# Kernel optimization log

Hardware: AMD Instinct MI355X
Metric: run time of the kernel (lower is better)

## Reference

```python
import jax, jax.numpy as jnp
import numpy as np

NUM_HEADS = 16
D_MODEL = 1024
D_K = D_MODEL // NUM_HEADS
B, S = 2, 2048


def setup_inputs() -> dict:
    key = jax.random.key(0)
    ks = jax.random.split(key, 10)
    q = jax.random.normal(ks[0], (B, S, D_MODEL), dtype=jnp.float32)
    k = jax.random.normal(ks[1], (B, S, D_MODEL), dtype=jnp.float32)
    v = jax.random.normal(ks[2], (B, S, D_MODEL), dtype=jnp.float32)
    # causal mask, 1 = keep, 0 = masked (masked_fill(mask==0, -1e9))
    mask = jnp.tril(jnp.ones((S, S), dtype=jnp.int32))[None, None, :, :]
    # Linear weights ~ N(0, 0.02); biases left at torch default-ish small uniform
    std = 0.02
    Wq = jax.random.normal(ks[3], (D_MODEL, D_MODEL), dtype=jnp.float32) * std
    Wk = jax.random.normal(ks[4], (D_MODEL, D_MODEL), dtype=jnp.float32) * std
    Wv = jax.random.normal(ks[5], (D_MODEL, D_MODEL), dtype=jnp.float32) * std
    bound = 1.0 / np.sqrt(D_MODEL)
    bq = jax.random.uniform(ks[6], (D_MODEL,), jnp.float32, -bound, bound)
    bk = jax.random.uniform(ks[7], (D_MODEL,), jnp.float32, -bound, bound)
    bv = jax.random.uniform(ks[8], (D_MODEL,), jnp.float32, -bound, bound)
    return {"q": q, "k": k, "v": v, "mask": mask,
            "Wq": Wq, "bq": bq, "Wk": Wk, "bk": bk, "Wv": Wv, "bv": bv}


def reference(q, k, v, mask, Wq, bq, Wk, bk, Wv, bv):
    # projections (torch Linear: x @ W.T + b), split heads -> [B, H, S, Dk]
    def proj(x, W, b):
        y = x @ W.T + b
        return y.reshape(B, S, NUM_HEADS, D_K).transpose(0, 2, 1, 3)

    qh, kh, vh = proj(q, Wq, bq), proj(k, Wk, bk), proj(v, Wv, bv)
    scores = jnp.einsum('bhqd,bhkd->bhqk', qh, kh) / jnp.sqrt(jnp.float32(D_K))
    scores = jnp.where(mask == 0, jnp.float32(-1e9), scores)
    p = jax.nn.softmax(scores, axis=-1)
    # dropout is identity in eval mode
    x = jnp.einsum('bhqk,bhkd->bhqd', p, vh)  # [B, H, S, Dk]
    return x.transpose(0, 2, 1, 3).reshape(B, S, D_MODEL)
```

## Files before the change

kernel.cpp:

```cpp
#include <hip/hip_runtime.h>

#define B_ 2
#define H_ 16
#define S_ 2048
#define DM 1024
#define DK 64
#define NX (4096 * 1024)
#define NW (1024 * 1024)
#define NO (32 * 2048 * 64)

typedef unsigned short u16;
typedef unsigned int u32;
typedef __attribute__((ext_vector_type(8))) short bf16x8;
typedef __attribute__((ext_vector_type(8))) unsigned short u16x8;
typedef __attribute__((ext_vector_type(4))) float f32x4;

__device__ inline u16 f2bf(float f) {
  union { float f; u32 u; } c; c.f = f;
  u32 u = c.u;
  u += 0x7fffu + ((u >> 16) & 1u);
  return (u16)(u >> 16);
}
__device__ inline float bf2f(u16 v) {
  union { u32 u; float f; } c; c.u = ((u32)v) << 16;
  return c.f;
}

__device__ inline u16x8 cvt8(const float* __restrict__ src) {
  const float4 a = *reinterpret_cast<const float4*>(src);
  const float4 b = *reinterpret_cast<const float4*>(src + 4);
  u16x8 r;
  r[0] = f2bf(a.x); r[1] = f2bf(a.y); r[2] = f2bf(a.z); r[3] = f2bf(a.w);
  r[4] = f2bf(b.x); r[5] = f2bf(b.y); r[6] = f2bf(b.z); r[7] = f2bf(b.w);
  return r;
}

__device__ inline void glds16(const u16* g, u16* l) {
  __builtin_amdgcn_global_load_lds(
      (const __attribute__((address_space(1))) unsigned int*)g,
      (__attribute__((address_space(3))) unsigned int*)l, 16, 0, 0);
}

__global__ __launch_bounds__(256) void cvt_kernel(
    const float* __restrict__ q, const float* __restrict__ k, const float* __restrict__ v,
    const float* __restrict__ Wq, const float* __restrict__ Wk, const float* __restrict__ Wv,
    u16* __restrict__ Xq, u16* __restrict__ Xk, u16* __restrict__ Xv,
    u16* __restrict__ Wqb, u16* __restrict__ Wkb, u16* __restrict__ Wvb)
{
  const int t = blockIdx.y;
  const float* src = (t == 0) ? q : (t == 1) ? k : (t == 2) ? v
                   : (t == 3) ? Wq : (t == 4) ? Wk : Wv;
  u16* dst = (t == 0) ? Xq : (t == 1) ? Xk : (t == 2) ? Xv
           : (t == 3) ? Wqb : (t == 4) ? Wkb : Wvb;
  const int n = (t < 3) ? NX : NW;
  const int idx = (blockIdx.x * 256 + threadIdx.x) * 8;
  if (idx >= n) return;
  *reinterpret_cast<u16x8*>(&dst[idx]) = cvt8(&src[idx]);
}

__global__ __launch_bounds__(256) void proj_kernel(
    const u16* __restrict__ Xq, const u16* __restrict__ Xk, const u16* __restrict__ Xv,
    const u16* __restrict__ Wqb, const u16* __restrict__ Wkb, const u16* __restrict__ Wvb,
    const float* __restrict__ bq, const float* __restrict__ bk, const float* __restrict__ bv,
    u16* __restrict__ Qh, u16* __restrict__ Kh, u16* __restrict__ Vh)
{
  const int z = blockIdx.z;
  const u16* X      = (z == 0) ? Xq : (z == 1) ? Xk : Xv;
  const u16* W      = (z == 0) ? Wqb : (z == 1) ? Wkb : Wvb;
  const float* bias = (z == 0) ? bq : (z == 1) ? bk : bv;
  u16* out          = (z == 0) ? Qh : (z == 1) ? Kh : Vh;
  const float scale = (z == 0) ? 0.18033688f : 1.0f;

  __shared__ __align__(16) u16 Xs[128 * 64];
  __shared__ __align__(16) u16 Ws[128 * 64];

  const int tid = threadIdx.x;
  const int lane = tid & 63;
  const int w = tid >> 6;
  const int wy = w >> 1, wx = w & 1;
  const int m0 = blockIdx.y * 128;
  const int n0 = blockIdx.x * 128;
  const int ml = lane & 15;
  const int qd = lane >> 4;

  f32x4 acc[4][4] = {};

  for (int kb = 0; kb < DM; kb += 64) {
    __syncthreads();
    #pragma unroll
    for (int p = 0; p < 4; ++p) {
      const int c = p * 4 + w;
      const int row = c * 8 + (lane >> 3);
      const int col = kb + (lane & 7) * 8;
      glds16(&X[(size_t)(m0 + row) * DM + col], &Xs[c * 512]);
      glds16(&W[(size_t)(n0 + row) * DM + col], &Ws[c * 512]);
    }
    __syncthreads();
    bf16x8 a[4][2], bfr[4][2];
    #pragma unroll
    for (int i = 0; i < 4; ++i)
      #pragma unroll
      for (int kc = 0; kc < 2; ++kc)
        a[i][kc] = *reinterpret_cast<const bf16x8*>(&Xs[(wy * 64 + i * 16 + ml) * 64 + kc * 32 + qd * 8]);
    #pragma unroll
    for (int j = 0; j < 4; ++j)
      #pragma unroll
      for (int kc = 0; kc < 2; ++kc)
        bfr[j][kc] = *reinterpret_cast<const bf16x8*>(&Ws[(wx * 64 + j * 16 + ml) * 64 + kc * 32 + qd * 8]);
    #pragma unroll
    for (int i = 0; i < 4; ++i)
      #pragma unroll
      for (int j = 0; j < 4; ++j) {
        acc[i][j] = __builtin_amdgcn_mfma_f32_16x16x32_bf16(a[i][0], bfr[j][0], acc[i][j], 0, 0, 0);
        acc[i][j] = __builtin_amdgcn_mfma_f32_16x16x32_bf16(a[i][1], bfr[j][1], acc[i][j], 0, 0, 0);
      }
  }

  #pragma unroll
  for (int j = 0; j < 4; ++j) {
    const int n = n0 + wx * 64 + j * 16 + ml;
    const float badd = bias[n];
    const int h = n >> 6, d = n & 63;
    #pragma unroll
    for (int i = 0; i < 4; ++i) {
      #pragma unroll
      for (int r = 0; r < 4; ++r) {
        const int m = m0 + wy * 64 + i * 16 + qd * 4 + r;
        const int bi = m >> 11, s = m & 2047;
        out[((bi * H_ + h) * S_ + s) * DK + d] = f2bf((acc[i][j][r] + badd) * scale);
      }
    }
  }
}

__global__ __launch_bounds__(256) void transpose_kernel(
    const u16* __restrict__ Vh, u16* __restrict__ Vt)
{
  __shared__ __align__(16) u16 T[64 * 72];
  const int t = threadIdx.x;
  const int st = blockIdx.x, bh = blockIdx.y;
  {
    const int r = t >> 2, c = (t & 3) * 16;
    const u16* src = &Vh[((size_t)bh * S_ + st * 64 + r) * DK + c];
    *reinterpret_cast<u16x8*>(&T[r * 72 + c])     = *reinterpret_cast<const u16x8*>(src);
    *reinterpret_cast<u16x8*>(&T[r * 72 + c + 8]) = *reinterpret_cast<const u16x8*>(src + 8);
  }
  __syncthreads();
  {
    const int d = t >> 2, s0 = (t & 3) * 16;
    u16x8 a, b;
    #pragma unroll
    for (int i = 0; i < 8; ++i) a[i] = T[(s0 + i) * 72 + d];
    #pragma unroll
    for (int i = 0; i < 8; ++i) b[i] = T[(s0 + 8 + i) * 72 + d];
    u16* dst = &Vt[((size_t)bh * DK + d) * S_ + st * 64 + s0];
    *reinterpret_cast<u16x8*>(dst)     = a;
    *reinterpret_cast<u16x8*>(dst + 8) = b;
  }
}

__global__ __launch_bounds__(256) void attn_kernel(
    const u16* __restrict__ Qh, const u16* __restrict__ Kh,
    const u16* __restrict__ Vt, u16* __restrict__ Op, float* __restrict__ lp)
{
  __shared__ __align__(16) u16 Ks[64 * 72];
  __shared__ __align__(16) u16 Vs[64 * 72];
  __shared__ __align__(16) u16 Ps[4 * 16 * 72];

  const int tid  = threadIdx.x;
  const int lane = tid & 63;
  const int w    = tid >> 6;
  const int qt   = 31 - blockIdx.x;
  const int bh   = blockIdx.y;
  const int half = blockIdx.z;
  const int nt   = qt + 1;
  const int na   = (nt + 1) >> 1;
  const int t0   = half ? na : 0;
  const int t1   = half ? nt : na;
  const int ml   = lane & 15, qd = lane >> 4;
  const int R0   = qt * 64 + w * 16;

  bf16x8 qa[2];
  #pragma unroll
  for (int ch = 0; ch < 2; ++ch)
    qa[ch] = *reinterpret_cast<const bf16x8*>(
        &Qh[((size_t)bh * S_ + R0 + ml) * DK + ch * 32 + qd * 8]);

  f32x4 oacc[4] = {};
  float l = 0.f;

  const u16* kbase = Kh + (size_t)bh * S_ * DK;
  const u16* vbase = Vt + (size_t)bh * DK * S_;
  u16* pw = &Ps[w * 16 * 72 + ml * 72];

  const int sr = tid >> 3;
  const int sc = (tid & 7) * 8;

  float4 kr0 = *reinterpret_cast<const float4*>(&kbase[(size_t)(t0 * 64 + sr) * DK + sc]);
  float4 kr1 = *reinterpret_cast<const float4*>(&kbase[(size_t)(t0 * 64 + sr + 32) * DK + sc]);
  float4 vr0 = *reinterpret_cast<const float4*>(&vbase[(size_t)sr * S_ + t0 * 64 + sc]);
  float4 vr1 = *reinterpret_cast<const float4*>(&vbase[(size_t)(sr + 32) * S_ + t0 * 64 + sc]);

  for (int t = t0; t < t1; ++t) {
    __syncthreads();
    *reinterpret_cast<float4*>(&Ks[sr * 72 + sc])        = kr0;
    *reinterpret_cast<float4*>(&Ks[(sr + 32) * 72 + sc]) = kr1;
    *reinterpret_cast<float4*>(&Vs[sr * 72 + sc])        = vr0;
    *reinterpret_cast<float4*>(&Vs[(sr + 32) * 72 + sc]) = vr1;
    __syncthreads();

    if (t + 1 < t1) {
      const int tn = t + 1;
      kr0 = *reinterpret_cast<const float4*>(&kbase[(size_t)(tn * 64 + sr) * DK + sc]);
      kr1 = *reinterpret_cast<const float4*>(&kbase[(size_t)(tn * 64 + sr + 32) * DK + sc]);
      vr0 = *reinterpret_cast<const float4*>(&vbase[(size_t)sr * S_ + tn * 64 + sc]);
      vr1 = *reinterpret_cast<const float4*>(&vbase[(size_t)(sr + 32) * S_ + tn * 64 + sc]);
    }

    const bool diag = (t == qt);
    const int jmax = diag ? w : 3;

    f32x4 sfr[4];
    #pragma unroll
    for (int j = 0; j < 4; ++j) {
      if (j > jmax) break;
      f32x4 zz = {};
      #pragma unroll
      for (int ch = 0; ch < 2; ++ch) {
        bf16x8 kb = *reinterpret_cast<const bf16x8*>(&Ks[(j * 16 + ml) * 72 + ch * 32 + qd * 8]);
        zz = __builtin_amdgcn_mfma_f32_16x16x32_bf16(kb, qa[ch], zz, 0, 0, 0);
      }
      sfr[j] = zz;
    }

    if (diag) {
      #pragma unroll
      for (int r = 0; r < 4; ++r)
        if (qd * 4 + r > ml) sfr[jmax][r] = -1e30f;
    }

    #pragma unroll
    for (int j = 0; j < 4; ++j) {
      u32 p0 = 0, p1 = 0;
      if (j <= jmax) {
        union { float f; u32 u; } e0, e1, e2, e3;
        e0.f = __builtin_amdgcn_exp2f(sfr[j][0]);
        e1.f = __builtin_amdgcn_exp2f(sfr[j][1]);
        e2.f = __builtin_amdgcn_exp2f(sfr[j][2]);
        e3.f = __builtin_amdgcn_exp2f(sfr[j][3]);
        l += (e0.f + e1.f) + (e2.f + e3.f);
        p0 = __builtin_amdgcn_perm(e1.u, e0.u, 0x07060302u);
        p1 = __builtin_amdgcn_perm(e3.u, e2.u, 0x07060302u);
      }
      u32* pd = reinterpret_cast<u32*>(&pw[j * 16 + qd * 4]);
      pd[0] = p0; pd[1] = p1;
    }

    const int chmax = (diag && w < 2) ? 0 : 1;
    #pragma unroll
    for (int ch = 0; ch < 2; ++ch) {
      if (ch > chmax) break;
      bf16x8 pa = *reinterpret_cast<const bf16x8*>(&Ps[w * 16 * 72 + ml * 72 + ch * 32 + qd * 8]);
      #pragma unroll
      for (int dj = 0; dj < 4; ++dj) {
        bf16x8 vb = *reinterpret_cast<const bf16x8*>(&Vs[(dj * 16 + ml) * 72 + ch * 32 + qd * 8]);
        oacc[dj] = __builtin_amdgcn_mfma_f32_16x16x32_bf16(pa, vb, oacc[dj], 0, 0, 0);
      }
    }
  }

  l += __shfl_xor(l, 16, 64);
  l += __shfl_xor(l, 32, 64);
  const size_t rbase = (size_t)(half * 32 + bh) * S_;
  if (qd == 0) lp[rbase + R0 + ml] = l;
  #pragma unroll
  for (int dj = 0; dj < 4; ++dj)
    #pragma unroll
    for (int r = 0; r < 4; ++r)
      Op[(rbase + R0 + qd * 4 + r) * DK + dj * 16 + ml] = f2bf(oacc[dj][r]);
}

__global__ __launch_bounds__(256) void merge_kernel(
    const u16* __restrict__ Op, const float* __restrict__ lp,
    float* __restrict__ out)
{
  const int idx8 = (blockIdx.x * 256 + threadIdx.x) * 8;
  const int row = idx8 >> 6;
  const int d = idx8 & 63;
  const float inv = 1.f / (lp[row] + lp[row + 32 * S_]);
  const u16x8 a = *reinterpret_cast<const u16x8*>(&Op[idx8]);
  const u16x8 c = *reinterpret_cast<const u16x8*>(&Op[(size_t)idx8 + NO]);
  const int bh = row >> 11, s = row & 2047;
  const int b = bh >> 4, h = bh & 15;
  float* dst = &out[(size_t)(b * S_ + s) * DM + h * DK + d];
  float4 o0, o1;
  o0.x = (bf2f(a[0]) + bf2f(c[0])) * inv;
  o0.y = (bf2f(a[1]) + bf2f(c[1])) * inv;
  o0.z = (bf2f(a[2]) + bf2f(c[2])) * inv;
  o0.w = (bf2f(a[3]) + bf2f(c[3])) * inv;
  o1.x = (bf2f(a[4]) + bf2f(c[4])) * inv;
  o1.y = (bf2f(a[5]) + bf2f(c[5])) * inv;
  o1.z = (bf2f(a[6]) + bf2f(c[6])) * inv;
  o1.w = (bf2f(a[7]) + bf2f(c[7])) * inv;
  *reinterpret_cast<float4*>(dst)     = o0;
  *reinterpret_cast<float4*>(dst + 4) = o1;
}

extern "C" void kernel_launch(void* const* d_in, const int* in_sizes, int n_in,
                              void* d_out, int out_size, void* d_ws, size_t ws_size,
                              hipStream_t stream) {
  const float* q  = (const float*)d_in[0];
  const float* k  = (const float*)d_in[1];
  const float* v  = (const float*)d_in[2];
  const float* Wq = (const float*)d_in[4];
  const float* bq = (const float*)d_in[5];
  const float* Wk = (const float*)d_in[6];
  const float* bk = (const float*)d_in[7];
  const float* Wv = (const float*)d_in[8];
  const float* bv = (const float*)d_in[9];

  u16* Xq  = (u16*)d_ws;
  u16* Xk  = Xq + NX;
  u16* Xv  = Xk + NX;
  u16* Wqb = Xv + NX;
  u16* Wkb = Wqb + NW;
  u16* Wvb = Wkb + NW;
  u16* Qh  = Wvb + NW;
  u16* Kh  = Qh + NX;
  u16* Vh  = Kh + NX;
  u16* Vt  = Xq;
  u16* Op  = Xk;
  float* lp = (float*)Wqb;

  cvt_kernel<<<dim3(NX / (256 * 8), 6), 256, 0, stream>>>(
      q, k, v, Wq, Wk, Wv, Xq, Xk, Xv, Wqb, Wkb, Wvb);
  proj_kernel<<<dim3(DM / 128, (B_ * S_) / 128, 3), 256, 0, stream>>>(
      Xq, Xk, Xv, Wqb, Wkb, Wvb, bq, bk, bv, Qh, Kh, Vh);
  transpose_kernel<<<dim3(S_ / 64, B_ * H_), 256, 0, stream>>>(Vh, Vt);
  attn_kernel<<<dim3(32, B_ * H_, 2), 256, 0, stream>>>(
      Qh, Kh, Vt, Op, lp);
  merge_kernel<<<NO / (256 * 8), 256, 0, stream>>>(Op, lp, (float*)d_out);
}
```

Baseline: 245.8 us.

## Process 128 query rows per attention block and shrink projection K-tile

The attention kernel now gives each block 128 query rows: each wave owns two 16-row m-tiles. Every K/V tile staged in shared memory therefore serves twice as many queries, and the grid is halved. Causal masking is generalised to per-m-tile edge checks with row-relative bounds. Separately, the projection GEMM steps K in chunks of 32 instead of 64, halving its LDS footprint at the cost of twice as many barriers and load phases.

```diff
diff --git a/kernel.cpp b/kernel.cpp
--- a/kernel.cpp
+++ b/kernel.cpp
@@ -71,8 +71,8 @@
   u16* out          = (z == 0) ? Qh : (z == 1) ? Kh : Vh;
   const float scale = (z == 0) ? 0.18033688f : 1.0f;
 
-  __shared__ __align__(16) u16 Xs[128 * 64];
-  __shared__ __align__(16) u16 Ws[128 * 64];
+  __shared__ __align__(16) u16 Xs[128 * 32];
+  __shared__ __align__(16) u16 Ws[128 * 32];
 
   const int tid = threadIdx.x;
   const int lane = tid & 63;
@@ -85,35 +85,29 @@
 
   f32x4 acc[4][4] = {};
 
-  for (int kb = 0; kb < DM; kb += 64) {
+  for (int kb = 0; kb < DM; kb += 32) {
     __syncthreads();
     #pragma unroll
-    for (int p = 0; p < 4; ++p) {
+    for (int p = 0; p < 2; ++p) {
       const int c = p * 4 + w;
-      const int row = c * 8 + (lane >> 3);
-      const int col = kb + (lane & 7) * 8;
+      const int row = c * 16 + (lane >> 2);
+      const int col = kb + (lane & 3) * 8;
       glds16(&X[(size_t)(m0 + row) * DM + col], &Xs[c * 512]);
       glds16(&W[(size_t)(n0 + row) * DM + col], &Ws[c * 512]);
     }
     __syncthreads();
-    bf16x8 a[4][2], bfr[4][2];
+    bf16x8 a[4], bfr[4];
     #pragma unroll
     for (int i = 0; i < 4; ++i)
-      #pragma unroll
-      for (int kc = 0; kc < 2; ++kc)
-        a[i][kc] = *reinterpret_cast<const bf16x8*>(&Xs[(wy * 64 + i * 16 + ml) * 64 + kc * 32 + qd * 8]);
+      a[i] = *reinterpret_cast<const bf16x8*>(&Xs[(wy * 64 + i * 16 + ml) * 32 + qd * 8]);
     #pragma unroll
     for (int j = 0; j < 4; ++j)
-      #pragma unroll
-      for (int kc = 0; kc < 2; ++kc)
-        bfr[j][kc] = *reinterpret_cast<const bf16x8*>(&Ws[(wx * 64 + j * 16 + ml) * 64 + kc * 32 + qd * 8]);
+      bfr[j] = *reinterpret_cast<const bf16x8*>(&Ws[(wx * 64 + j * 16 + ml) * 32 + qd * 8]);
     #pragma unroll
     for (int i = 0; i < 4; ++i)
       #pragma unroll
-      for (int j = 0; j < 4; ++j) {
-        acc[i][j] = __builtin_amdgcn_mfma_f32_16x16x32_bf16(a[i][0], bfr[j][0], acc[i][j], 0, 0, 0);
-        acc[i][j] = __builtin_amdgcn_mfma_f32_16x16x32_bf16(a[i][1], bfr[j][1], acc[i][j], 0, 0, 0);
-      }
+      for (int j = 0; j < 4; ++j)
+        acc[i][j] = __builtin_amdgcn_mfma_f32_16x16x32_bf16(a[i], bfr[j], acc[i][j], 0, 0, 0);
   }
 
   #pragma unroll
@@ -170,24 +164,26 @@
   const int tid  = threadIdx.x;
   const int lane = tid & 63;
   const int w    = tid >> 6;
-  const int qt   = 31 - blockIdx.x;
+  const int qt   = 15 - blockIdx.x;
   const int bh   = blockIdx.y;
   const int half = blockIdx.z;
-  const int nt   = qt + 1;
-  const int na   = (nt + 1) >> 1;
+  const int nt   = 2 * (qt + 1);
+  const int na   = qt + 1;
   const int t0   = half ? na : 0;
   const int t1   = half ? nt : na;
   const int ml   = lane & 15, qd = lane >> 4;
-  const int R0   = qt * 64 + w * 16;
-
-  bf16x8 qa[2];
+  const int R0b  = qt * 128 + w * 32;
+
+  bf16x8 qa[2][2];
   #pragma unroll
-  for (int ch = 0; ch < 2; ++ch)
-    qa[ch] = *reinterpret_cast<const bf16x8*>(
-        &Qh[((size_t)bh * S_ + R0 + ml) * DK + ch * 32 + qd * 8]);
-
-  f32x4 oacc[4] = {};
-  float l = 0.f;
+  for (int mt = 0; mt < 2; ++mt)
+    #pragma unroll
+    for (int ch = 0; ch < 2; ++ch)
+      qa[mt][ch] = *reinterpret_cast<const bf16x8*>(
+          &Qh[((size_t)bh * S_ + R0b + mt * 16 + ml) * DK + ch * 32 + qd * 8]);
+
+  f32x4 oacc[2][4] = {};
+  float lsum[2] = {0.f, 0.f};
 
   const u16* kbase = Kh + (size_t)bh * S_ * DK;
   const u16* vbase = Vt + (size_t)bh * DK * S_;
@@ -217,67 +213,82 @@
       vr1 = *reinterpret_cast<const float4*>(&vbase[(size_t)(sr + 32) * S_ + tn * 64 + sc]);
     }
 
-    const bool diag = (t == qt);
-    const int jmax = diag ? w : 3;
-
-    f32x4 sfr[4];
-    #pragma unroll
-    for (int j = 0; j < 4; ++j) {
-      if (j > jmax) break;
-      f32x4 zz = {};
+    #pragma unroll
+    for (int mt = 0; mt < 2; ++mt) {
+      const int R0 = R0b + mt * 16;
+      const int rel = R0 + 15 - t * 64;
+      if (rel < 0) continue;
+      const int jmax = (rel >> 4) > 3 ? 3 : (rel >> 4);
+      const bool edge = (t * 64 + 63 > R0);
+
+      f32x4 sfr[4];
+      #pragma unroll
+      for (int j = 0; j < 4; ++j) {
+        if (j > jmax) break;
+        f32x4 zz = {};
+        #pragma unroll
+        for (int ch = 0; ch < 2; ++ch) {
+          bf16x8 kb = *reinterpret_cast<const bf16x8*>(&Ks[(j * 16 + ml) * 72 + ch * 32 + qd * 8]);
+          zz = __builtin_amdgcn_mfma_f32_16x16x32_bf16(kb, qa[mt][ch], zz, 0, 0, 0);
+        }
+        sfr[j] = zz;
+      }
+
+      if (edge) {
+        #pragma unroll
+        for (int j = 0; j < 4; ++j) {
+          if (j > jmax) break;
+          #pragma unroll
+          for (int r = 0; r < 4; ++r)
+            if (t * 64 + j * 16 + qd * 4 + r > R0 + ml) sfr[j][r] = -1e30f;
+        }
+      }
+
+      #pragma unroll
+      for (int j = 0; j < 4; ++j) {
+        u32 p0 = 0, p1 = 0;
+        if (j <= jmax) {
+          union { float f; u32 u; } e0, e1, e2, e3;
+          e0.f = __builtin_amdgcn_exp2f(sfr[j][0]);
+          e1.f = __builtin_amdgcn_exp2f(sfr[j][1]);
+          e2.f = __builtin_amdgcn_exp2f(sfr[j][2]);
+          e3.f = __builtin_amdgcn_exp2f(sfr[j][3]);
+          lsum[mt] += (e0.f + e1.f) + (e2.f + e3.f);
+          p0 = __builtin_amdgcn_perm(e1.u, e0.u, 0x07060302u);
+          p1 = __builtin_amdgcn_perm(e3.u, e2.u, 0x07060302u);
+        }
+        u32* pd = reinterpret_cast<u32*>(&pw[j * 16 + qd * 4]);
+        pd[0] = p0; pd[1] = p1;
+      }
+
+      const int chmax = jmax >> 1;
       #pragma unroll
       for (int ch = 0; ch < 2; ++ch) {
-        bf16x8 kb = *reinterpret_cast<const bf16x8*>(&Ks[(j * 16 + ml) * 72 + ch * 32 + qd * 8]);
-        zz = __builtin_amdgcn_mfma_f32_16x16x32_bf16(kb, qa[ch], zz, 0, 0, 0);
-      }
-      sfr[j] = zz;
+        if (ch > chmax) break;
+        bf16x8 pa = *reinterpret_cast<const bf16x8*>(&Ps[w * 16 * 72 + ml * 72 + ch * 32 + qd * 8]);
+        #pragma unroll
+        for (int dj = 0; dj < 4; ++dj) {
+          bf16x8 vb = *reinterpret_cast<const bf16x8*>(&Vs[(dj * 16 + ml) * 72 + ch * 32 + qd * 8]);
+          oacc[mt][dj] = __builtin_amdgcn_mfma_f32_16x16x32_bf16(pa, vb, oacc[mt][dj], 0, 0, 0);
+        }
+      }
     }
-
-    if (diag) {
+  }
+
+  const size_t rbase = (size_t)(half * 32 + bh) * S_;
+  #pragma unroll
+  for (int mt = 0; mt < 2; ++mt) {
+    float lm = lsum[mt];
+    lm += __shfl_xor(lm, 16, 64);
+    lm += __shfl_xor(lm, 32, 64);
+    const int R0 = R0b + mt * 16;
+    if (qd == 0) lp[rbase + R0 + ml] = lm;
+    #pragma unroll
+    for (int dj = 0; dj < 4; ++dj)
       #pragma unroll
       for (int r = 0; r < 4; ++r)
-        if (qd * 4 + r > ml) sfr[jmax][r] = -1e30f;
-    }
-
-    #pragma unroll
-    for (int j = 0; j < 4; ++j) {
-      u32 p0 = 0, p1 = 0;
-      if (j <= jmax) {
-        union { float f; u32 u; } e0, e1, e2, e3;
-        e0.f = __builtin_amdgcn_exp2f(sfr[j][0]);
-        e1.f = __builtin_amdgcn_exp2f(sfr[j][1]);
-        e2.f = __builtin_amdgcn_exp2f(sfr[j][2]);
-        e3.f = __builtin_amdgcn_exp2f(sfr[j][3]);
-        l += (e0.f + e1.f) + (e2.f + e3.f);
-        p0 = __builtin_amdgcn_perm(e1.u, e0.u, 0x07060302u);
-        p1 = __builtin_amdgcn_perm(e3.u, e2.u, 0x07060302u);
-      }
-      u32* pd = reinterpret_cast<u32*>(&pw[j * 16 + qd * 4]);
-      pd[0] = p0; pd[1] = p1;
-    }
-
-    const int chmax = (diag && w < 2) ? 0 : 1;
-    #pragma unroll
-    for (int ch = 0; ch < 2; ++ch) {
-      if (ch > chmax) break;
-      bf16x8 pa = *reinterpret_cast<const bf16x8*>(&Ps[w * 16 * 72 + ml * 72 + ch * 32 + qd * 8]);
-      #pragma unroll
-      for (int dj = 0; dj < 4; ++dj) {
-        bf16x8 vb = *reinterpret_cast<const bf16x8*>(&Vs[(dj * 16 + ml) * 72 + ch * 32 + qd * 8]);
-        oacc[dj] = __builtin_amdgcn_mfma_f32_16x16x32_bf16(pa, vb, oacc[dj], 0, 0, 0);
-      }
-    }
-  }
-
-  l += __shfl_xor(l, 16, 64);
-  l += __shfl_xor(l, 32, 64);
-  const size_t rbase = (size_t)(half * 32 + bh) * S_;
-  if (qd == 0) lp[rbase + R0 + ml] = l;
-  #pragma unroll
-  for (int dj = 0; dj < 4; ++dj)
-    #pragma unroll
-    for (int r = 0; r < 4; ++r)
-      Op[(rbase + R0 + qd * 4 + r) * DK + dj * 16 + ml] = f2bf(oacc[dj][r]);
+        Op[(rbase + R0 + qd * 4 + r) * DK + dj * 16 + ml] = f2bf(oacc[mt][dj][r]);
+  }
 }
 
 __global__ __launch_bounds__(256) void merge_kernel(
@@ -337,7 +348,7 @@
   proj_kernel<<<dim3(DM / 128, (B_ * S_) / 128, 3), 256, 0, stream>>>(
       Xq, Xk, Xv, Wqb, Wkb, Wvb, bq, bk, bv, Qh, Kh, Vh);
   transpose_kernel<<<dim3(S_ / 64, B_ * H_), 256, 0, stream>>>(Vh, Vt);
-  attn_kernel<<<dim3(32, B_ * H_, 2), 256, 0, stream>>>(
+  attn_kernel<<<dim3(16, B_ * H_, 2), 256, 0, stream>>>(
       Qh, Kh, Vt, Op, lp);
   merge_kernel<<<NO / (256 * 8), 256, 0, stream>>>(Op, lp, (float*)d_out);
 }
```

Result: faster. 238.9 us (-2.8%).
